# Optimization experiments

Measured on AMD Instinct MI355X. Metric: run time of the kernel, lower is better.

The kernel has to match this reference:

```python
import jax, jax.numpy as jnp
import numpy as np

B, T, D = 256, 261, 768      # batch, tokens (1 cls + 4 reg + 16*16 patches), embed_dim
NUM_REG = 4
G = 16                       # patch grid side = 224 // 14
ROI = 3                      # roi_side


def setup_inputs() -> dict:
    key = jax.random.key(0)
    k1, k2 = jax.random.split(key)
    tokens = jax.random.normal(k1, (B, T, D), jnp.float32)
    W_proj = jax.random.normal(k2, (D, D), jnp.float32) * (1.0 / np.sqrt(D))
    b_proj = jnp.zeros((D,), jnp.float32)
    return {"tokens": tokens, "W_proj": W_proj, "b_proj": b_proj}


def _buddy_pool_all(cues, patches2d):
    # cues: [B, C, d]; patches2d: [B, H, W, d]
    Bn, H, W, d = patches2d.shape
    flat = patches2d.reshape(Bn, H * W, d)
    sim = jnp.einsum('bcd,bnd->bcn', cues, flat)          # [B, C, HW]
    idx = jnp.argmax(sim, axis=-1)                         # [B, C]
    h, w = idx // W, idx % W
    r = ROI // 2
    rows = jnp.arange(H)
    cols = jnp.arange(W)
    # clipped ROI window == torch slice(max(0,h-r), min(H,h+r+1)) as a mask
    rmask = (rows[None, None, :] >= (h - r)[..., None]) & (rows[None, None, :] <= (h + r)[..., None])  # [B,C,H]
    cmask = (cols[None, None, :] >= (w - r)[..., None]) & (cols[None, None, :] <= (w + r)[..., None])  # [B,C,W]
    mask = (rmask[..., :, None] & cmask[..., None, :]).astype(patches2d.dtype)  # [B,C,H,W]
    roi_sum = jnp.einsum('bchw,bhwd->bcd', mask, patches2d)
    cnt = jnp.sum(mask, axis=(-2, -1))[..., None]          # 4, 6, or 9 at borders
    return roi_sum / cnt                                   # [B, C, d]


def reference(tokens, W_proj, b_proj):
    t = tokens @ W_proj.T + b_proj                         # nn.Linear projection
    cues = t[:, : 1 + NUM_REG, :]                          # cls + registers: [B,5,d]
    patches2d = t[:, 1 + NUM_REG :, :].reshape(t.shape[0], G, G, D)
    rois = _buddy_pool_all(cues, patches2d)                # [B,5,d]
    toks = jnp.concatenate([cues, rois], axis=1)           # [B,10,d]
    n = jnp.linalg.norm(toks, axis=-1, keepdims=True)
    return toks / jnp.maximum(n, 1e-12)                    # F.normalize
```

## Files before the change

kernel.cpp:

```cpp
#include <hip/hip_runtime.h>
#include <math.h>

constexpr int kB = 256;
constexpr int kT = 261;
constexpr int kD = 768;
constexpr int kC = 5;
constexpr int kG = 16;
constexpr int kP = 256;
constexpr int kTok = kT * kD;
constexpr float kTau = 0.03f;
constexpr int kSlots = 64;

typedef short short8v __attribute__((ext_vector_type(8)));
typedef float f32x4 __attribute__((ext_vector_type(4)));
typedef unsigned short ushort_t;

__device__ inline ushort_t f2bf(float x) {
    unsigned int u = __float_as_uint(x);
    unsigned int r = (u + 0x7FFFu + ((u >> 16) & 1u)) >> 16;
    return (ushort_t)r;
}
__device__ inline float bf2f(ushort_t h) { return __uint_as_float(((unsigned int)h) << 16); }


__global__ __launch_bounds__(256)
void kprep(const float* __restrict__ W,
           ushort_t* __restrict__ Wb_hi, ushort_t* __restrict__ Wb_lo,
           ushort_t* __restrict__ Wt_hi, ushort_t* __restrict__ Wt_lo)
{
    __shared__ ushort_t Lhi[32][36], Llo[32][36];
    const int blk = blockIdx.x, tr = blk / 24, tc = blk % 24;
    const int t = threadIdx.x, r = t >> 3, q = t & 7;
    const int row = tr * 32 + r, col = tc * 32 + q * 4;
    const float4 v = *(const float4*)&W[(size_t)row * kD + col];
    const ushort_t h0 = f2bf(v.x), h1 = f2bf(v.y), h2 = f2bf(v.z), h3 = f2bf(v.w);
    const ushort_t l0 = f2bf(v.x - bf2f(h0)), l1 = f2bf(v.y - bf2f(h1));
    const ushort_t l2 = f2bf(v.z - bf2f(h2)), l3 = f2bf(v.w - bf2f(h3));
    *(ushort4*)&Wb_hi[(size_t)row * kD + col] = make_ushort4(h0, h1, h2, h3);
    *(ushort4*)&Wb_lo[(size_t)row * kD + col] = make_ushort4(l0, l1, l2, l3);
    Lhi[r][q*4+0] = h0; Lhi[r][q*4+1] = h1; Lhi[r][q*4+2] = h2; Lhi[r][q*4+3] = h3;
    Llo[r][q*4+0] = l0; Llo[r][q*4+1] = l1; Llo[r][q*4+2] = l2; Llo[r][q*4+3] = l3;
    __syncthreads();
    const size_t orow = (size_t)(tc * 32 + r) * kD + tr * 32 + q * 4;
    *(ushort4*)&Wt_hi[orow] = make_ushort4(Lhi[q*4+0][r], Lhi[q*4+1][r], Lhi[q*4+2][r], Lhi[q*4+3][r]);
    *(ushort4*)&Wt_lo[orow] = make_ushort4(Llo[q*4+0][r], Llo[q*4+1][r], Llo[q*4+2][r], Llo[q*4+3][r]);
}

template<int MODE>
__global__ __launch_bounds__(256)
void kmm(const float* __restrict__ tokens,
         const ushort_t* __restrict__ Bhi, const ushort_t* __restrict__ Blo,
         const float* __restrict__ bvec, const float* __restrict__ Asrc,
         float* __restrict__ dstA, float* __restrict__ dstB)
{
    __shared__ ushort_t Ah[32][40], Al[32][40];
    __shared__ ushort_t Bh[64][40], Bl[64][40];
    const int mt = blockIdx.x, nt = blockIdx.y, t = threadIdx.x;
    const int w = t >> 6, l = t & 63;
    const int ln = l & 15, kq = l >> 4;
    const int mf = w & 1, nh = w >> 1;
    const int ar = t >> 3, aq = t & 7;
    const int br = t >> 2, bq = t & 3;

    const int am = mt * 32 + ar;
    const float* __restrict__ Ap = (MODE == 0) ? tokens : Asrc;
    const size_t arow = (MODE == 0)
        ? ((size_t)(am / 5) * kTok + (size_t)(am % 5) * kD)
        : ((size_t)am * kD);
    const size_t brow = (size_t)(nt * 64 + br) * kD;

    float4 pa; uint4 pbh, pbl;
    auto load_regs = [&](int kc) {
        pa  = *(const float4*)&Ap[arow + kc + aq * 4];
        pbh = *(const uint4*)&Bhi[brow + kc + bq * 8];
        pbl = *(const uint4*)&Blo[brow + kc + bq * 8];
    };
    auto write_lds = [&]() {
        const ushort_t h0 = f2bf(pa.x), h1 = f2bf(pa.y), h2 = f2bf(pa.z), h3 = f2bf(pa.w);
        const ushort_t a0 = f2bf(pa.x - bf2f(h0)), a1 = f2bf(pa.y - bf2f(h1));
        const ushort_t a2 = f2bf(pa.z - bf2f(h2)), a3 = f2bf(pa.w - bf2f(h3));
        *(ushort4*)&Ah[ar][aq * 4] = make_ushort4(h0, h1, h2, h3);
        *(ushort4*)&Al[ar][aq * 4] = make_ushort4(a0, a1, a2, a3);
        *(uint4*)&Bh[br][bq * 8] = pbh;
        *(uint4*)&Bl[br][bq * 8] = pbl;
    };

    f32x4 acc0 = {0.f, 0.f, 0.f, 0.f}, acc1 = {0.f, 0.f, 0.f, 0.f};
    auto compute = [&]() {
        const short8v ah  = *(const short8v*)&Ah[mf * 16 + ln][kq * 8];
        const short8v al_ = *(const short8v*)&Al[mf * 16 + ln][kq * 8];
        const short8v bh0 = *(const short8v*)&Bh[nh * 32 + ln][kq * 8];
        const short8v bl0 = *(const short8v*)&Bl[nh * 32 + ln][kq * 8];
        const short8v bh1 = *(const short8v*)&Bh[nh * 32 + 16 + ln][kq * 8];
        const short8v bl1 = *(const short8v*)&Bl[nh * 32 + 16 + ln][kq * 8];
        acc0 = __builtin_amdgcn_mfma_f32_16x16x32_bf16(al_, bh0, acc0, 0, 0, 0);
        acc0 = __builtin_amdgcn_mfma_f32_16x16x32_bf16(ah,  bl0, acc0, 0, 0, 0);
        acc0 = __builtin_amdgcn_mfma_f32_16x16x32_bf16(ah,  bh0, acc0, 0, 0, 0);
        acc1 = __builtin_amdgcn_mfma_f32_16x16x32_bf16(al_, bh1, acc1, 0, 0, 0);
        acc1 = __builtin_amdgcn_mfma_f32_16x16x32_bf16(ah,  bl1, acc1, 0, 0, 0);
        acc1 = __builtin_amdgcn_mfma_f32_16x16x32_bf16(ah,  bh1, acc1, 0, 0, 0);
    };

    load_regs(0);
    write_lds();
    __syncthreads();
    for (int kc = 32; kc < kD; kc += 32) {
        load_regs(kc);
        compute();
        __syncthreads();
        write_lds();
        __syncthreads();
    }
    compute();

    #pragma unroll
    for (int nf = 0; nf < 2; ++nf) {
        const int col = nt * 64 + nh * 32 + nf * 16 + ln;
        const float bb = (MODE != 1) ? bvec[col] : 0.f;
        const f32x4 acc = nf ? acc1 : acc0;
        #pragma unroll
        for (int r = 0; r < 4; ++r) {
            const int row = mt * 32 + mf * 16 + kq * 4 + r;
            const float val = acc[r] + bb;
            if (MODE == 0) {
                dstA[(size_t)row * kD + col] = val;
                dstB[((size_t)(row / 5) * 10 + (row % 5)) * kD + col] = val;
            } else if (MODE == 1) {
                dstA[(size_t)row * kD + col] = val;
            } else {
                dstA[((size_t)(row / 5) * 10 + 5 + (row % 5)) * kD + col] = val;
            }
        }
    }
}

__global__ __launch_bounds__(256)
void ksim(const float* __restrict__ tokens, const float* __restrict__ u_all,
          float* __restrict__ simsp)
{
    __shared__ ushort_t Uh[6][392], Ul[6][392];
    const int b = blockIdx.x, pq = blockIdx.y, kh = blockIdx.z;
    const int t = threadIdx.x;
    const int w = t >> 6, lane = t & 63;
    const int ln = lane & 15, kq = lane >> 4;
    const size_t tb = (size_t)b * kTok;

    for (int i = t; i < 384; i += 256) {
        const int gd = kh * 384 + i;
        #pragma unroll
        for (int c = 0; c < kC; ++c) {
            const float v = u_all[(size_t)b * kC * kD + (size_t)c * kD + gd];
            const ushort_t h = f2bf(v);
            Uh[c][i] = h; Ul[c][i] = f2bf(v - bf2f(h));
        }
        Uh[kC][i] = 0; Ul[kC][i] = 0;
    }
    __syncthreads();

    const int urow = (ln < kC) ? ln : kC;
    const int n0 = pq * 64 + w * 16;
    const float* __restrict__ prow =
        &tokens[tb + (size_t)(kC + n0 + ln) * kD + kh * 384 + kq * 8];

    f32x4 acc = {0.f, 0.f, 0.f, 0.f};
    #pragma unroll
    for (int c = 0; c < 12; ++c) {
        const float4 fa = *(const float4*)&prow[c * 32];
        const float4 fb = *(const float4*)&prow[c * 32 + 4];
        const float fv[8] = {fa.x, fa.y, fa.z, fa.w, fb.x, fb.y, fb.z, fb.w};
        short8v bh, bl;
        #pragma unroll
        for (int j = 0; j < 8; ++j) {
            const ushort_t h = f2bf(fv[j]);
            bh[j] = (short)h;
            bl[j] = (short)f2bf(fv[j] - bf2f(h));
        }
        const short8v ah  = *(const short8v*)&Uh[urow][c * 32 + kq * 8];
        const short8v al_ = *(const short8v*)&Ul[urow][c * 32 + kq * 8];
        acc = __builtin_amdgcn_mfma_f32_16x16x32_bf16(al_, bh, acc, 0, 0, 0);
        acc = __builtin_amdgcn_mfma_f32_16x16x32_bf16(ah,  bl, acc, 0, 0, 0);
        acc = __builtin_amdgcn_mfma_f32_16x16x32_bf16(ah,  bh, acc, 0, 0, 0);
    }
    float* __restrict__ sp = simsp + (size_t)kh * (1280 * (size_t)kP);
    const int n = n0 + ln;
    if (kq == 0) {
        #pragma unroll
        for (int r = 0; r < 4; ++r)
            sp[((size_t)b * kC + r) * kP + n] = acc[r];
    } else if (kq == 1) {
        sp[((size_t)b * kC + 4) * kP + n] = acc[0];
    }
}

__global__ __launch_bounds__(64)
void ktop(const float* __restrict__ simsp, int* __restrict__ bestn, int* __restrict__ flagw)
{
    const int pair = blockIdx.x;
    const int lane = threadIdx.x;
    const float* s0 = &simsp[(size_t)pair * kP];
    const float* s1 = &simsp[1280 * (size_t)kP + (size_t)pair * kP];
    float m1 = -3.4e38f, m2 = -3.4e38f; int i1 = 0;
    #pragma unroll
    for (int k = 0; k < 4; ++k) {
        const int n = lane + k * 64;
        const float v = s0[n] + s1[n];
        if (v > m1 || (v == m1 && n < i1)) { m2 = m1; m1 = v; i1 = n; }
        else if (v > m2) m2 = v;
    }
    #pragma unroll
    for (int off = 32; off >= 1; off >>= 1) {
        const float om1 = __shfl_xor(m1, off, 64);
        const int   oi1 = __shfl_xor(i1, off, 64);
        const float om2 = __shfl_xor(m2, off, 64);
        float nm2 = fmaxf(m2, om2);
        if (om1 > m1 || (om1 == m1 && oi1 < i1)) { nm2 = fmaxf(nm2, m1); m1 = om1; i1 = oi1; }
        else nm2 = fmaxf(nm2, om1);
        m2 = nm2;
    }
    if (lane == 0) {
        bestn[pair] = i1;
        flagw[pair] = (m1 - m2 < kTau) ? 1 : 0;
    }
}

__global__ __launch_bounds__(256)
void kcompact(const int* __restrict__ flagw, int* __restrict__ cnt, int* __restrict__ flist)
{
    __shared__ int scnt;
    const int t = threadIdx.x;
    if (t == 0) scnt = 0;
    __syncthreads();
    for (int p = t; p < 1280; p += 256)
        if (flagw[p]) { const int i = atomicAdd(&scnt, 1); if (i < kSlots) flist[i] = p; }
    __syncthreads();
    if (t == 0) *cnt = min(scnt, kSlots);
}

__global__ __launch_bounds__(256)
void kr_tcb(const float* __restrict__ tokens, const float* __restrict__ W,
            const float* __restrict__ bvec, const int* __restrict__ cnt,
            const int* __restrict__ flist, double* __restrict__ tcb64g)
{
    const int slot = blockIdx.x;
    if (slot >= *cnt) return;
    const int pair = flist[slot];
    const int b = pair / 5, c = pair % 5;
    const int js = blockIdx.y;
    const int t = threadIdx.x, w = t >> 6, lane = t & 63;
    const size_t tb = (size_t)b * kTok;

    const float* cuep = &tokens[tb + (size_t)c * kD + lane * 4];
    const float4 cf0 = *(const float4*)&cuep[0];
    const float4 cf1 = *(const float4*)&cuep[256];
    const float4 cf2 = *(const float4*)&cuep[512];
    for (int it = 0; it < 16; ++it) {
        const int j = js * 64 + it * 4 + w;
        const float* wr = &W[(size_t)j * kD + lane * 4];
        const float4 w0 = *(const float4*)&wr[0];
        const float4 w1 = *(const float4*)&wr[256];
        const float4 w2 = *(const float4*)&wr[512];
        double acc = (double)w0.x*cf0.x + (double)w0.y*cf0.y + (double)w0.z*cf0.z + (double)w0.w*cf0.w
                   + (double)w1.x*cf1.x + (double)w1.y*cf1.y + (double)w1.z*cf1.z + (double)w1.w*cf1.w
                   + (double)w2.x*cf2.x + (double)w2.y*cf2.y + (double)w2.z*cf2.z + (double)w2.w*cf2.w;
        #pragma unroll
        for (int off = 32; off >= 1; off >>= 1)
            acc += __shfl_xor(acc, off, 64);
        if (lane == 0) tcb64g[(size_t)slot * kD + j] = acc + (double)bvec[j];
    }
}

__global__ __launch_bounds__(256)
void kr_u(const float* __restrict__ W, const int* __restrict__ cnt,
          const double* __restrict__ tcb64g, double* __restrict__ u64g)
{
    const int slot = blockIdx.x;
    if (slot >= *cnt) return;
    __shared__ double part[4][64];
    const int t = threadIdx.x;
    const int i = t & 63, jq = t >> 6;
    const int i0 = blockIdx.y * 64;

    const double* tc = &tcb64g[(size_t)slot * kD + jq * 192];
    const float* wp = &W[(size_t)(jq * 192) * kD + i0 + i];
    double acc = 0.0;
    #pragma unroll 8
    for (int j = 0; j < 192; ++j)
        acc += tc[j] * (double)wp[(size_t)j * kD];
    part[jq][i] = acc;
    __syncthreads();
    if (t < 64)
        u64g[(size_t)slot * kD + i0 + t] = part[0][t] + part[1][t] + part[2][t] + part[3][t];
}

__global__ __launch_bounds__(256)
void kr_sim(const float* __restrict__ tokens, const int* __restrict__ cnt,
            const int* __restrict__ flist, const double* __restrict__ u64g,
            double* __restrict__ s64g)
{
    const int slot = blockIdx.x;
    if (slot >= *cnt) return;
    __shared__ double u64s[kD];
    const int pair = flist[slot];
    const int b = pair / 5;
    const int ps = blockIdx.y;
    const int t = threadIdx.x, w = t >> 6, lane = t & 63;
    const size_t tb = (size_t)b * kTok;

    u64s[t]       = u64g[(size_t)slot * kD + t];
    u64s[t + 256] = u64g[(size_t)slot * kD + t + 256];
    u64s[t + 512] = u64g[(size_t)slot * kD + t + 512];
    __syncthreads();

    #pragma unroll
    for (int it = 0; it < 8; ++it) {
        const int n = ps * 32 + w * 8 + it;
        const float* p = &tokens[tb + (size_t)(kC + n) * kD + lane * 4];
        const float4 p0 = *(const float4*)&p[0];
        const float4 p1 = *(const float4*)&p[256];
        const float4 p2 = *(const float4*)&p[512];
        const double* ud = &u64s[lane * 4];
        double acc = (double)p0.x*ud[0]   + (double)p0.y*ud[1]   + (double)p0.z*ud[2]   + (double)p0.w*ud[3]
                   + (double)p1.x*ud[256] + (double)p1.y*ud[257] + (double)p1.z*ud[258] + (double)p1.w*ud[259]
                   + (double)p2.x*ud[512] + (double)p2.y*ud[513] + (double)p2.z*ud[514] + (double)p2.w*ud[515];
        #pragma unroll
        for (int off = 32; off >= 1; off >>= 1)
            acc += __shfl_xor(acc, off, 64);
        if (lane == 0) s64g[(size_t)slot * kP + n] = acc;
    }
}

__global__ __launch_bounds__(64)
void kr_arg(const int* __restrict__ cnt, const int* __restrict__ flist,
            const double* __restrict__ s64g, int* __restrict__ bestn)
{
    const int slot = blockIdx.x;
    if (slot >= *cnt) return;
    const int lane = threadIdx.x;
    const double* s = &s64g[(size_t)slot * kP];
    double best = -1.0e300; int bi = 0;
    #pragma unroll
    for (int k = 0; k < 4; ++k) {
        const int n = lane + k * 64;
        const double v = s[n];
        if (v > best || (v == best && n < bi)) { best = v; bi = n; }
    }
    #pragma unroll
    for (int off = 32; off >= 1; off >>= 1) {
        const double v2 = __shfl_xor(best, off, 64);
        const int    i2 = __shfl_xor(bi, off, 64);
        if (v2 > best || (v2 == best && i2 < bi)) { best = v2; bi = i2; }
    }
    if (lane == 0) bestn[flist[slot]] = bi;
}

__global__ __launch_bounds__(256)
void kroi(const float* __restrict__ tokens, const int* __restrict__ bestn,
          float* __restrict__ roi)
{
    const int b = blockIdx.x, c = blockIdx.y, t = threadIdx.x;
    const size_t tb = (size_t)b * kTok;
    const int nn = bestn[b * kC + c];
    const int h = nn >> 4, ww = nn & 15;
    const int rlo = max(h - 1, 0), rhi = min(h + 1, kG - 1);
    const int clo = max(ww - 1, 0), chi = min(ww + 1, kG - 1);
    const float inv = 1.0f / (float)((rhi - rlo + 1) * (chi - clo + 1));
    #pragma unroll
    for (int s = 0; s < 3; ++s) {
        const int d = t + s * 256;
        float sum = 0.f;
        for (int rr = rlo; rr <= rhi; ++rr)
            for (int cc = clo; cc <= chi; ++cc)
                sum += tokens[tb + (size_t)(kC + rr * kG + cc) * kD + d];
        roi[((size_t)b * kC + c) * kD + d] = sum * inv;
    }
}

__global__ __launch_bounds__(256)
void knorm(float* __restrict__ out)
{
    __shared__ float wsum[4];
    const int row = blockIdx.x, t = threadIdx.x;
    float* p = out + (size_t)row * kD;
    const float x0 = p[t], x1 = p[t + 256], x2 = p[t + 512];
    float ss = x0 * x0 + x1 * x1 + x2 * x2;
    #pragma unroll
    for (int off = 32; off >= 1; off >>= 1) ss += __shfl_down(ss, off, 64);
    if ((t & 63) == 0) wsum[t >> 6] = ss;
    __syncthreads();
    const float tot = wsum[0] + wsum[1] + wsum[2] + wsum[3];
    const float nrm = fmaxf(sqrtf(tot), 1e-12f);
    p[t] = x0 / nrm; p[t + 256] = x1 / nrm; p[t + 512] = x2 / nrm;
}

extern "C" void kernel_launch(void* const* d_in, const int* in_sizes, int n_in,
                              void* d_out, int out_size, void* d_ws, size_t ws_size,
                              hipStream_t stream) {
    const float* tokens = (const float*)d_in[0];
    const float* W      = (const float*)d_in[1];
    const float* bvec   = (const float*)d_in[2];
    float* out = (float*)d_out;
    float* ws = (float*)d_ws;
    float* simsp = ws;
    float* tcb   = ws;
    float* u_all = ws + 983040;
    float* roi   = ws + 1966080;
    int*   bestn = (int*)(ws + 2949120);
    int*   flagw = (int*)(ws + 2950400);
    ushort_t* wsb = (ushort_t*)(ws + 2951680);
    ushort_t* Wb_hi = wsb;
    ushort_t* Wb_lo = wsb + 589824;
    ushort_t* Wt_hi = wsb + 1179648;
    ushort_t* Wt_lo = wsb + 1769472;
    int*    cnt    = (int*)(ws + 4131328);
    int*    flist  = (int*)(ws + 4131329);
    double* tcb64g = (double*)(ws + 4131400);
    double* u64g   = (double*)(ws + 4229704);
    double* s64g   = (double*)(ws + 4328008);

    kprep<<<dim3(576), 256, 0, stream>>>(W, Wb_hi, Wb_lo, Wt_hi, Wt_lo);
    kmm<0><<<dim3(40, 12), 256, 0, stream>>>(tokens, Wb_hi, Wb_lo, bvec, nullptr, tcb, out);
    kmm<1><<<dim3(40, 12), 256, 0, stream>>>(tokens, Wt_hi, Wt_lo, bvec, tcb, u_all, nullptr);
    ksim<<<dim3(256, 4, 2), 256, 0, stream>>>(tokens, u_all, simsp);
    ktop<<<dim3(1280), 64, 0, stream>>>(simsp, bestn, flagw);
    kcompact<<<dim3(1), 256, 0, stream>>>(flagw, cnt, flist);
    kr_tcb<<<dim3(kSlots, 12), 256, 0, stream>>>(tokens, W, bvec, cnt, flist, tcb64g);
    kr_u<<<dim3(kSlots, 12), 256, 0, stream>>>(W, cnt, tcb64g, u64g);
    kr_sim<<<dim3(kSlots, 8), 256, 0, stream>>>(tokens, cnt, flist, u64g, s64g);
    kr_arg<<<dim3(kSlots), 64, 0, stream>>>(cnt, flist, s64g, bestn);
    kroi<<<dim3(256, 5), 256, 0, stream>>>(tokens, bestn, roi);
    kmm<2><<<dim3(40, 12), 256, 0, stream>>>(tokens, Wb_hi, Wb_lo, bvec, roi, out, nullptr);
    knorm<<<dim3(2560), 256, 0, stream>>>(out);
}
```

Before: 152.5 us.

## Load GEMM fragments directly from global memory and fold compaction into top-2 kernel

The small GEMM kernel (kmm) no longer stages A and B tiles through LDS with barriers. Each lane now loads its MFMA fragments straight from global memory and splits A into hi/lo bf16 in registers, fully unrolled over K. Separately, the single-block compaction kernel is removed: ktop appends ambiguous pairs to a list with a global atomic, and a memset clears the counter first. This saves LDS round-trips, barriers and one launch, at the cost of redundant global/L2 loads across waves and a nondeterministic order in the flagged list.

```diff
diff --git a/kernel.cpp b/kernel.cpp
--- a/kernel.cpp
+++ b/kernel.cpp
@@ -53,65 +53,48 @@
          const float* __restrict__ bvec, const float* __restrict__ Asrc,
          float* __restrict__ dstA, float* __restrict__ dstB)
 {
-    __shared__ ushort_t Ah[32][40], Al[32][40];
-    __shared__ ushort_t Bh[64][40], Bl[64][40];
     const int mt = blockIdx.x, nt = blockIdx.y, t = threadIdx.x;
     const int w = t >> 6, l = t & 63;
     const int ln = l & 15, kq = l >> 4;
     const int mf = w & 1, nh = w >> 1;
-    const int ar = t >> 3, aq = t & 7;
-    const int br = t >> 2, bq = t & 3;
-
-    const int am = mt * 32 + ar;
+
+    const int am = mt * 32 + mf * 16 + ln;
     const float* __restrict__ Ap = (MODE == 0) ? tokens : Asrc;
     const size_t arow = (MODE == 0)
         ? ((size_t)(am / 5) * kTok + (size_t)(am % 5) * kD)
         : ((size_t)am * kD);
-    const size_t brow = (size_t)(nt * 64 + br) * kD;
-
-    float4 pa; uint4 pbh, pbl;
-    auto load_regs = [&](int kc) {
-        pa  = *(const float4*)&Ap[arow + kc + aq * 4];
-        pbh = *(const uint4*)&Bhi[brow + kc + bq * 8];
-        pbl = *(const uint4*)&Blo[brow + kc + bq * 8];
-    };
-    auto write_lds = [&]() {
-        const ushort_t h0 = f2bf(pa.x), h1 = f2bf(pa.y), h2 = f2bf(pa.z), h3 = f2bf(pa.w);
-        const ushort_t a0 = f2bf(pa.x - bf2f(h0)), a1 = f2bf(pa.y - bf2f(h1));
-        const ushort_t a2 = f2bf(pa.z - bf2f(h2)), a3 = f2bf(pa.w - bf2f(h3));
-        *(ushort4*)&Ah[ar][aq * 4] = make_ushort4(h0, h1, h2, h3);
-        *(ushort4*)&Al[ar][aq * 4] = make_ushort4(a0, a1, a2, a3);
-        *(uint4*)&Bh[br][bq * 8] = pbh;
-        *(uint4*)&Bl[br][bq * 8] = pbl;
-    };
+    const float* __restrict__ aptr = &Ap[arow + kq * 8];
+
+    const size_t b0row = (size_t)(nt * 64 + nh * 32 + ln) * kD + kq * 8;
+    const ushort_t* __restrict__ bh0p = &Bhi[b0row];
+    const ushort_t* __restrict__ bl0p = &Blo[b0row];
+    const ushort_t* __restrict__ bh1p = &Bhi[b0row + 16 * (size_t)kD];
+    const ushort_t* __restrict__ bl1p = &Blo[b0row + 16 * (size_t)kD];
 
     f32x4 acc0 = {0.f, 0.f, 0.f, 0.f}, acc1 = {0.f, 0.f, 0.f, 0.f};
-    auto compute = [&]() {
-        const short8v ah  = *(const short8v*)&Ah[mf * 16 + ln][kq * 8];
-        const short8v al_ = *(const short8v*)&Al[mf * 16 + ln][kq * 8];
-        const short8v bh0 = *(const short8v*)&Bh[nh * 32 + ln][kq * 8];
-        const short8v bl0 = *(const short8v*)&Bl[nh * 32 + ln][kq * 8];
-        const short8v bh1 = *(const short8v*)&Bh[nh * 32 + 16 + ln][kq * 8];
-        const short8v bl1 = *(const short8v*)&Bl[nh * 32 + 16 + ln][kq * 8];
+    #pragma unroll
+    for (int c = 0; c < 24; ++c) {
+        const float4 fa0 = *(const float4*)&aptr[c * 32];
+        const float4 fa1 = *(const float4*)&aptr[c * 32 + 4];
+        const float fv[8] = {fa0.x, fa0.y, fa0.z, fa0.w, fa1.x, fa1.y, fa1.z, fa1.w};
+        short8v ah, al_;
+        #pragma unroll
+        for (int j = 0; j < 8; ++j) {
+            const ushort_t h = f2bf(fv[j]);
+            ah[j]  = (short)h;
+            al_[j] = (short)f2bf(fv[j] - bf2f(h));
+        }
+        const short8v bh0 = *(const short8v*)&bh0p[c * 32];
+        const short8v bl0 = *(const short8v*)&bl0p[c * 32];
+        const short8v bh1 = *(const short8v*)&bh1p[c * 32];
+        const short8v bl1 = *(const short8v*)&bl1p[c * 32];
         acc0 = __builtin_amdgcn_mfma_f32_16x16x32_bf16(al_, bh0, acc0, 0, 0, 0);
         acc0 = __builtin_amdgcn_mfma_f32_16x16x32_bf16(ah,  bl0, acc0, 0, 0, 0);
         acc0 = __builtin_amdgcn_mfma_f32_16x16x32_bf16(ah,  bh0, acc0, 0, 0, 0);
         acc1 = __builtin_amdgcn_mfma_f32_16x16x32_bf16(al_, bh1, acc1, 0, 0, 0);
         acc1 = __builtin_amdgcn_mfma_f32_16x16x32_bf16(ah,  bl1, acc1, 0, 0, 0);
         acc1 = __builtin_amdgcn_mfma_f32_16x16x32_bf16(ah,  bh1, acc1, 0, 0, 0);
-    };
-
-    load_regs(0);
-    write_lds();
-    __syncthreads();
-    for (int kc = 32; kc < kD; kc += 32) {
-        load_regs(kc);
-        compute();
-        __syncthreads();
-        write_lds();
-        __syncthreads();
-    }
-    compute();
+    }
 
     #pragma unroll
     for (int nf = 0; nf < 2; ++nf) {
@@ -193,7 +176,8 @@
 }
 
 __global__ __launch_bounds__(64)
-void ktop(const float* __restrict__ simsp, int* __restrict__ bestn, int* __restrict__ flagw)
+void ktop(const float* __restrict__ simsp, int* __restrict__ bestn,
+          int* __restrict__ cnt, int* __restrict__ flist)
 {
     const int pair = blockIdx.x;
     const int lane = threadIdx.x;
@@ -219,21 +203,11 @@
     }
     if (lane == 0) {
         bestn[pair] = i1;
-        flagw[pair] = (m1 - m2 < kTau) ? 1 : 0;
-    }
-}
-
-__global__ __launch_bounds__(256)
-void kcompact(const int* __restrict__ flagw, int* __restrict__ cnt, int* __restrict__ flist)
-{
-    __shared__ int scnt;
-    const int t = threadIdx.x;
-    if (t == 0) scnt = 0;
-    __syncthreads();
-    for (int p = t; p < 1280; p += 256)
-        if (flagw[p]) { const int i = atomicAdd(&scnt, 1); if (i < kSlots) flist[i] = p; }
-    __syncthreads();
-    if (t == 0) *cnt = min(scnt, kSlots);
+        if (m1 - m2 < kTau) {
+            const int i = atomicAdd(cnt, 1);
+            if (i < kSlots) flist[i] = pair;
+        }
+    }
 }
 
 __global__ __launch_bounds__(256)
@@ -242,7 +216,7 @@
             const int* __restrict__ flist, double* __restrict__ tcb64g)
 {
     const int slot = blockIdx.x;
-    if (slot >= *cnt) return;
+    if (slot >= min(*cnt, kSlots)) return;
     const int pair = flist[slot];
     const int b = pair / 5, c = pair % 5;
     const int js = blockIdx.y;
@@ -274,7 +248,7 @@
           const double* __restrict__ tcb64g, double* __restrict__ u64g)
 {
     const int slot = blockIdx.x;
-    if (slot >= *cnt) return;
+    if (slot >= min(*cnt, kSlots)) return;
     __shared__ double part[4][64];
     const int t = threadIdx.x;
     const int i = t & 63, jq = t >> 6;
@@ -298,7 +272,7 @@
             double* __restrict__ s64g)
 {
     const int slot = blockIdx.x;
-    if (slot >= *cnt) return;
+    if (slot >= min(*cnt, kSlots)) return;
     __shared__ double u64s[kD];
     const int pair = flist[slot];
     const int b = pair / 5;
@@ -334,7 +308,7 @@
             const double* __restrict__ s64g, int* __restrict__ bestn)
 {
     const int slot = blockIdx.x;
-    if (slot >= *cnt) return;
+    if (slot >= min(*cnt, kSlots)) return;
     const int lane = threadIdx.x;
     const double* s = &s64g[(size_t)slot * kP];
     double best = -1.0e300; int bi = 0;
@@ -405,7 +379,6 @@
     float* u_all = ws + 983040;
     float* roi   = ws + 1966080;
     int*   bestn = (int*)(ws + 2949120);
-    int*   flagw = (int*)(ws + 2950400);
     ushort_t* wsb = (ushort_t*)(ws + 2951680);
     ushort_t* Wb_hi = wsb;
     ushort_t* Wb_lo = wsb + 589824;
@@ -417,12 +390,12 @@
     double* u64g   = (double*)(ws + 4229704);
     double* s64g   = (double*)(ws + 4328008);
 
+    hipMemsetAsync(cnt, 0, sizeof(int), stream);
     kprep<<<dim3(576), 256, 0, stream>>>(W, Wb_hi, Wb_lo, Wt_hi, Wt_lo);
     kmm<0><<<dim3(40, 12), 256, 0, stream>>>(tokens, Wb_hi, Wb_lo, bvec, nullptr, tcb, out);
     kmm<1><<<dim3(40, 12), 256, 0, stream>>>(tokens, Wt_hi, Wt_lo, bvec, tcb, u_all, nullptr);
     ksim<<<dim3(256, 4, 2), 256, 0, stream>>>(tokens, u_all, simsp);
-    ktop<<<dim3(1280), 64, 0, stream>>>(simsp, bestn, flagw);
-    kcompact<<<dim3(1), 256, 0, stream>>>(flagw, cnt, flist);
+    ktop<<<dim3(1280), 64, 0, stream>>>(simsp, bestn, cnt, flist);
     kr_tcb<<<dim3(kSlots, 12), 256, 0, stream>>>(tokens, W, bvec, cnt, flist, tcb64g);
     kr_u<<<dim3(kSlots, 12), 256, 0, stream>>>(W, cnt, tcb64g, u64g);
     kr_sim<<<dim3(kSlots, 8), 256, 0, stream>>>(tokens, cnt, flist, u64g, s64g);
```

New measurement: 205.1 us. 1.34x slower.

## Halve GEMM N-tile to double block count and fold flag compaction into ktop

Applied to the files above, without the earlier changes.

The kmm GEMM tile shrinks from 32x64 to 32x32, so each wave computes one 16x16 fragment and the grid doubles to 40x24 blocks. This spreads the small M=1280 GEMMs over more of the GPU's compute units. The cost is more A-tile reloads and bf16 split conversion per output. Separately, the single-block kcompact launch is removed: ktop atomically appends ambiguous pairs to the list directly, with the counter zeroed by a memset and later kernels clamping it to kSlots. The list order becomes nondeterministic.

```diff
diff --git a/kernel.cpp b/kernel.cpp
--- a/kernel.cpp
+++ b/kernel.cpp
@@ -54,26 +54,26 @@
          float* __restrict__ dstA, float* __restrict__ dstB)
 {
     __shared__ ushort_t Ah[32][40], Al[32][40];
-    __shared__ ushort_t Bh[64][40], Bl[64][40];
+    __shared__ ushort_t Bh[32][40], Bl[32][40];
     const int mt = blockIdx.x, nt = blockIdx.y, t = threadIdx.x;
     const int w = t >> 6, l = t & 63;
     const int ln = l & 15, kq = l >> 4;
-    const int mf = w & 1, nh = w >> 1;
+    const int mf = w & 1, nf = w >> 1;
     const int ar = t >> 3, aq = t & 7;
-    const int br = t >> 2, bq = t & 3;
+    const int br = t >> 3, bq = t & 7;
 
     const int am = mt * 32 + ar;
     const float* __restrict__ Ap = (MODE == 0) ? tokens : Asrc;
     const size_t arow = (MODE == 0)
         ? ((size_t)(am / 5) * kTok + (size_t)(am % 5) * kD)
         : ((size_t)am * kD);
-    const size_t brow = (size_t)(nt * 64 + br) * kD;
-
-    float4 pa; uint4 pbh, pbl;
+    const size_t brow = (size_t)(nt * 32 + br) * kD;
+
+    float4 pa; ushort4 pbh, pbl;
     auto load_regs = [&](int kc) {
         pa  = *(const float4*)&Ap[arow + kc + aq * 4];
-        pbh = *(const uint4*)&Bhi[brow + kc + bq * 8];
-        pbl = *(const uint4*)&Blo[brow + kc + bq * 8];
+        pbh = *(const ushort4*)&Bhi[brow + kc + bq * 4];
+        pbl = *(const ushort4*)&Blo[brow + kc + bq * 4];
     };
     auto write_lds = [&]() {
         const ushort_t h0 = f2bf(pa.x), h1 = f2bf(pa.y), h2 = f2bf(pa.z), h3 = f2bf(pa.w);
@@ -81,24 +81,19 @@
         const ushort_t a2 = f2bf(pa.z - bf2f(h2)), a3 = f2bf(pa.w - bf2f(h3));
         *(ushort4*)&Ah[ar][aq * 4] = make_ushort4(h0, h1, h2, h3);
         *(ushort4*)&Al[ar][aq * 4] = make_ushort4(a0, a1, a2, a3);
-        *(uint4*)&Bh[br][bq * 8] = pbh;
-        *(uint4*)&Bl[br][bq * 8] = pbl;
+        *(ushort4*)&Bh[br][bq * 4] = pbh;
+        *(ushort4*)&Bl[br][bq * 4] = pbl;
     };
 
-    f32x4 acc0 = {0.f, 0.f, 0.f, 0.f}, acc1 = {0.f, 0.f, 0.f, 0.f};
+    f32x4 acc = {0.f, 0.f, 0.f, 0.f};
     auto compute = [&]() {
         const short8v ah  = *(const short8v*)&Ah[mf * 16 + ln][kq * 8];
         const short8v al_ = *(const short8v*)&Al[mf * 16 + ln][kq * 8];
-        const short8v bh0 = *(const short8v*)&Bh[nh * 32 + ln][kq * 8];
-        const short8v bl0 = *(const short8v*)&Bl[nh * 32 + ln][kq * 8];
-        const short8v bh1 = *(const short8v*)&Bh[nh * 32 + 16 + ln][kq * 8];
-        const short8v bl1 = *(const short8v*)&Bl[nh * 32 + 16 + ln][kq * 8];
-        acc0 = __builtin_amdgcn_mfma_f32_16x16x32_bf16(al_, bh0, acc0, 0, 0, 0);
-        acc0 = __builtin_amdgcn_mfma_f32_16x16x32_bf16(ah,  bl0, acc0, 0, 0, 0);
-        acc0 = __builtin_amdgcn_mfma_f32_16x16x32_bf16(ah,  bh0, acc0, 0, 0, 0);
-        acc1 = __builtin_amdgcn_mfma_f32_16x16x32_bf16(al_, bh1, acc1, 0, 0, 0);
-        acc1 = __builtin_amdgcn_mfma_f32_16x16x32_bf16(ah,  bl1, acc1, 0, 0, 0);
-        acc1 = __builtin_amdgcn_mfma_f32_16x16x32_bf16(ah,  bh1, acc1, 0, 0, 0);
+        const short8v bh  = *(const short8v*)&Bh[nf * 16 + ln][kq * 8];
+        const short8v bl  = *(const short8v*)&Bl[nf * 16 + ln][kq * 8];
+        acc = __builtin_amdgcn_mfma_f32_16x16x32_bf16(al_, bh, acc, 0, 0, 0);
+        acc = __builtin_amdgcn_mfma_f32_16x16x32_bf16(ah,  bl, acc, 0, 0, 0);
+        acc = __builtin_amdgcn_mfma_f32_16x16x32_bf16(ah,  bh, acc, 0, 0, 0);
     };
 
     load_regs(0);
@@ -113,23 +108,19 @@
     }
     compute();
 
-    #pragma unroll
-    for (int nf = 0; nf < 2; ++nf) {
-        const int col = nt * 64 + nh * 32 + nf * 16 + ln;
-        const float bb = (MODE != 1) ? bvec[col] : 0.f;
-        const f32x4 acc = nf ? acc1 : acc0;
-        #pragma unroll
-        for (int r = 0; r < 4; ++r) {
-            const int row = mt * 32 + mf * 16 + kq * 4 + r;
-            const float val = acc[r] + bb;
-            if (MODE == 0) {
-                dstA[(size_t)row * kD + col] = val;
-                dstB[((size_t)(row / 5) * 10 + (row % 5)) * kD + col] = val;
-            } else if (MODE == 1) {
-                dstA[(size_t)row * kD + col] = val;
-            } else {
-                dstA[((size_t)(row / 5) * 10 + 5 + (row % 5)) * kD + col] = val;
-            }
+    const int col = nt * 32 + nf * 16 + ln;
+    const float bb = (MODE != 1) ? bvec[col] : 0.f;
+    #pragma unroll
+    for (int r = 0; r < 4; ++r) {
+        const int row = mt * 32 + mf * 16 + kq * 4 + r;
+        const float val = acc[r] + bb;
+        if (MODE == 0) {
+            dstA[(size_t)row * kD + col] = val;
+            dstB[((size_t)(row / 5) * 10 + (row % 5)) * kD + col] = val;
+        } else if (MODE == 1) {
+            dstA[(size_t)row * kD + col] = val;
+        } else {
+            dstA[((size_t)(row / 5) * 10 + 5 + (row % 5)) * kD + col] = val;
         }
     }
 }
@@ -193,7 +184,8 @@
 }
 
 __global__ __launch_bounds__(64)
-void ktop(const float* __restrict__ simsp, int* __restrict__ bestn, int* __restrict__ flagw)
+void ktop(const float* __restrict__ simsp, int* __restrict__ bestn,
+          int* __restrict__ cnt, int* __restrict__ flist)
 {
     const int pair = blockIdx.x;
     const int lane = threadIdx.x;
@@ -219,21 +211,11 @@
     }
     if (lane == 0) {
         bestn[pair] = i1;
-        flagw[pair] = (m1 - m2 < kTau) ? 1 : 0;
-    }
-}
-
-__global__ __launch_bounds__(256)
-void kcompact(const int* __restrict__ flagw, int* __restrict__ cnt, int* __restrict__ flist)
-{
-    __shared__ int scnt;
-    const int t = threadIdx.x;
-    if (t == 0) scnt = 0;
-    __syncthreads();
-    for (int p = t; p < 1280; p += 256)
-        if (flagw[p]) { const int i = atomicAdd(&scnt, 1); if (i < kSlots) flist[i] = p; }
-    __syncthreads();
-    if (t == 0) *cnt = min(scnt, kSlots);
+        if (m1 - m2 < kTau) {
+            const int i = atomicAdd(cnt, 1);
+            if (i < kSlots) flist[i] = pair;
+        }
+    }
 }
 
 __global__ __launch_bounds__(256)
@@ -242,7 +224,7 @@
             const int* __restrict__ flist, double* __restrict__ tcb64g)
 {
     const int slot = blockIdx.x;
-    if (slot >= *cnt) return;
+    if (slot >= min(*cnt, kSlots)) return;
     const int pair = flist[slot];
     const int b = pair / 5, c = pair % 5;
     const int js = blockIdx.y;
@@ -274,7 +256,7 @@
           const double* __restrict__ tcb64g, double* __restrict__ u64g)
 {
     const int slot = blockIdx.x;
-    if (slot >= *cnt) return;
+    if (slot >= min(*cnt, kSlots)) return;
     __shared__ double part[4][64];
     const int t = threadIdx.x;
     const int i = t & 63, jq = t >> 6;
@@ -298,7 +280,7 @@
             double* __restrict__ s64g)
 {
     const int slot = blockIdx.x;
-    if (slot >= *cnt) return;
+    if (slot >= min(*cnt, kSlots)) return;
     __shared__ double u64s[kD];
     const int pair = flist[slot];
     const int b = pair / 5;
@@ -334,7 +316,7 @@
             const double* __restrict__ s64g, int* __restrict__ bestn)
 {
     const int slot = blockIdx.x;
-    if (slot >= *cnt) return;
+    if (slot >= min(*cnt, kSlots)) return;
     const int lane = threadIdx.x;
     const double* s = &s64g[(size_t)slot * kP];
     double best = -1.0e300; int bi = 0;
@@ -405,7 +387,6 @@
     float* u_all = ws + 983040;
     float* roi   = ws + 1966080;
     int*   bestn = (int*)(ws + 2949120);
-    int*   flagw = (int*)(ws + 2950400);
     ushort_t* wsb = (ushort_t*)(ws + 2951680);
     ushort_t* Wb_hi = wsb;
     ushort_t* Wb_lo = wsb + 589824;
@@ -417,17 +398,17 @@
     double* u64g   = (double*)(ws + 4229704);
     double* s64g   = (double*)(ws + 4328008);
 
+    hipMemsetAsync(cnt, 0, sizeof(int), stream);
     kprep<<<dim3(576), 256, 0, stream>>>(W, Wb_hi, Wb_lo, Wt_hi, Wt_lo);
-    kmm<0><<<dim3(40, 12), 256, 0, stream>>>(tokens, Wb_hi, Wb_lo, bvec, nullptr, tcb, out);
-    kmm<1><<<dim3(40, 12), 256, 0, stream>>>(tokens, Wt_hi, Wt_lo, bvec, tcb, u_all, nullptr);
+    kmm<0><<<dim3(40, 24), 256, 0, stream>>>(tokens, Wb_hi, Wb_lo, bvec, nullptr, tcb, out);
+    kmm<1><<<dim3(40, 24), 256, 0, stream>>>(tokens, Wt_hi, Wt_lo, bvec, tcb, u_all, nullptr);
     ksim<<<dim3(256, 4, 2), 256, 0, stream>>>(tokens, u_all, simsp);
-    ktop<<<dim3(1280), 64, 0, stream>>>(simsp, bestn, flagw);
-    kcompact<<<dim3(1), 256, 0, stream>>>(flagw, cnt, flist);
+    ktop<<<dim3(1280), 64, 0, stream>>>(simsp, bestn, cnt, flist);
     kr_tcb<<<dim3(kSlots, 12), 256, 0, stream>>>(tokens, W, bvec, cnt, flist, tcb64g);
     kr_u<<<dim3(kSlots, 12), 256, 0, stream>>>(W, cnt, tcb64g, u64g);
     kr_sim<<<dim3(kSlots, 8), 256, 0, stream>>>(tokens, cnt, flist, u64g, s64g);
     kr_arg<<<dim3(kSlots), 64, 0, stream>>>(cnt, flist, s64g, bestn);
     kroi<<<dim3(256, 5), 256, 0, stream>>>(tokens, bestn, roi);
-    kmm<2><<<dim3(40, 12), 256, 0, stream>>>(tokens, Wb_hi, Wb_lo, bvec, roi, out, nullptr);
+    kmm<2><<<dim3(40, 24), 256, 0, stream>>>(tokens, Wb_hi, Wb_lo, bvec, roi, out, nullptr);
     knorm<<<dim3(2560), 256, 0, stream>>>(out);
 }
```

Result: no change. 152.3 us (-0.1%).
